# Performance work log

Measured on AMD Instinct MI355X. Metric: run time of the kernel, lower is better.

The kernel has to match this reference:

```python
import jax, jax.numpy as jnp
import numpy as np

B, S, H, E, V, T, OOV = 32, 400, 256, 300, 50000, 20, 50


def setup_inputs() -> dict:
    key = jax.random.key(0)
    ks = jax.random.split(key, 24)
    g = lambda k, sh, scale=0.02: jax.random.normal(k, sh, dtype=jnp.float32) * scale
    return {
        "enc_hidden": jax.random.normal(ks[0], (B, S, 2 * H), dtype=jnp.float32),
        "h0": jax.random.normal(ks[1], (B, H), dtype=jnp.float32),
        "c0": jax.random.normal(ks[2], (B, H), dtype=jnp.float32),
        "embedding": g(ks[3], (V, E), 1.0),
        "W_enc": g(ks[4], (2 * H, H)),
        "W_dec": g(ks[5], (H, H)),
        "w_cov": g(ks[6], (H,)),
        "v_attn": g(ks[7], (H,)),
        "W_ih": g(ks[8], (E, 4 * H)),
        "W_hh": g(ks[9], (H, 4 * H)),
        "b_lstm": jnp.zeros((4 * H,), jnp.float32),
        "W_out1": g(ks[10], (3 * H, H)),
        "b_out1": jnp.zeros((H,), jnp.float32),
        "W_out2": g(ks[11], (H, V)),
        "b_out2": jnp.zeros((V,), jnp.float32),
        "w_h": g(ks[12], (2 * H, 1)),
        "w_s": g(ks[13], (H, 1)),
        "w_x": g(ks[14], (E, 1)),
        "b_x": jnp.zeros((1,), jnp.float32),
        "dec_input": jax.random.randint(ks[15], (B, T), 0, V),
        "enc_input_ext": jax.random.randint(ks[16], (B, S), 0, V + OOV),
        "enc_pad_mask": jnp.ones((B, S), dtype=bool),
        "max_oov_len": OOV,
    }


def reference(enc_hidden, h0, c0, embedding, W_enc, W_dec, w_cov, v_attn,
              W_ih, W_hh, b_lstm, W_out1, b_out1, W_out2, b_out2,
              w_h, w_s, w_x, b_x, dec_input, enc_input_ext, enc_pad_mask,
              max_oov_len):
    b, s, two_h = enc_hidden.shape
    enc_feat = enc_hidden @ W_enc  # [B,S,H], precomputed attention keys
    batch_idx = jnp.arange(b)[:, None]
    NEG = jnp.float32(-1e9)

    def step(carry, x_t):
        h, c, cov = carry
        emb = embedding[x_t]  # [B,E]
        # LSTM cell
        gates = emb @ W_ih + h @ W_hh + b_lstm
        i, f, gg, o = jnp.split(gates, 4, axis=-1)
        c = jax.nn.sigmoid(f) * c + jax.nn.sigmoid(i) * jnp.tanh(gg)
        h = jax.nn.sigmoid(o) * jnp.tanh(c)
        # coverage attention over encoder states
        e = jnp.tanh(enc_feat + (h @ W_dec)[:, None, :] + cov[..., None] * w_cov) @ v_attn  # [B,S]
        e = jnp.where(enc_pad_mask, e, NEG)
        attn = jax.nn.softmax(e, axis=-1)
        context = jnp.einsum('bs,bsd->bd', attn, enc_hidden)  # [B,2H]
        cov = cov + attn
        # vocab distribution
        out = jnp.concatenate([h, context], axis=-1) @ W_out1 + b_out1
        vocab_dist = jax.nn.softmax(out @ W_out2 + b_out2, axis=-1)  # [B,V]
        # pointer-generator gate
        p_gen = jax.nn.sigmoid(context @ w_h + h @ w_s + emb @ w_x + b_x)  # [B,1]
        vocab_dist = p_gen * vocab_dist
        weighted_attn = (1.0 - p_gen) * attn
        # extend vocab and scatter-add copy probabilities
        ext = jnp.concatenate(
            [vocab_dist, jnp.zeros((b, max_oov_len), vocab_dist.dtype)], axis=-1)
        final = ext.at[batch_idx, enc_input_ext].add(weighted_attn)
        return (h, c, cov), (final, attn, cov)

    cov0 = jnp.zeros((b, s), jnp.float32)
    _, (finals, attns, covs) = jax.lax.scan(step, (h0, c0, cov0), dec_input.T)
    # stack with time on the last axis, as in the torch module
    return (jnp.moveaxis(finals, 0, -1),
            jnp.moveaxis(attns, 0, -1),
            jnp.moveaxis(covs, 0, -1))
```

## Files before the change

kernel.cpp:

```cpp
#include <hip/hip_runtime.h>
#include <hip/hip_bf16.h>

#define B_    32
#define S_    400
#define H_    256
#define E_    300
#define V_    50000
#define T_    20
#define VE_   50050
#define TB_   640
#define VPAD_ 50048
#define FIN_  32032000
#define NB_   16
#define SC_   25

typedef __attribute__((ext_vector_type(8))) short bf16x8;
typedef __attribute__((ext_vector_type(4))) float f32x4;

__device__ __forceinline__ float sigmoid_f(float x){ return 1.f/(1.f+__expf(-x)); }
__device__ __forceinline__ float tanh_f(float x){ return 1.f - 2.f/(__expf(2.f*x)+1.f); }

__device__ __forceinline__ float bf2f(unsigned short u){
  union { unsigned int i; float f; } x; x.i = ((unsigned int)u) << 16; return x.f;
}
__device__ __forceinline__ unsigned short f2bf(float f){
  union { __hip_bfloat16 h; unsigned short u; } x; x.h = __float2bfloat16(f); return x.u;
}

__device__ __forceinline__ void st_dev(float* p, float v){
  __hip_atomic_store(p, v, __ATOMIC_RELAXED, __HIP_MEMORY_SCOPE_AGENT);
}
__device__ __forceinline__ float ld_dev(const float* p){
  return __hip_atomic_load(p, __ATOMIC_RELAXED, __HIP_MEMORY_SCOPE_AGENT);
}

__device__ __forceinline__ void rowbar(int* cnt, int* gen, int target){
  __syncthreads();
  if (threadIdx.x == 0){
    asm volatile("s_waitcnt vmcnt(0)" ::: "memory");
    int old = __hip_atomic_fetch_add(cnt, 1, __ATOMIC_RELAXED, __HIP_MEMORY_SCOPE_AGENT);
    if (old == NB_ - 1){
      __hip_atomic_store(cnt, 0, __ATOMIC_RELAXED, __HIP_MEMORY_SCOPE_AGENT);
      asm volatile("s_waitcnt vmcnt(0)" ::: "memory");
      __hip_atomic_fetch_add(gen, 1, __ATOMIC_RELAXED, __HIP_MEMORY_SCOPE_AGENT);
    } else {
      while (__hip_atomic_load(gen, __ATOMIC_RELAXED, __HIP_MEMORY_SCOPE_AGENT) < target){
        __builtin_amdgcn_s_sleep(1);
      }
    }
  }
  __syncthreads();
}


__global__ __launch_bounds__(256) void kc1(const float* __restrict__ in,
                                           __hip_bfloat16* __restrict__ out){
  size_t g = (size_t)blockIdx.x*256 + threadIdx.x;
  float4 f = ((const float4*)in)[g];
  size_t o = g*4;
  out[o+0] = __float2bfloat16(f.x);
  out[o+1] = __float2bfloat16(f.y);
  out[o+2] = __float2bfloat16(f.z);
  out[o+3] = __float2bfloat16(f.w);
}

__global__ __launch_bounds__(256) void kT(const float* __restrict__ in,
                                          __hip_bfloat16* __restrict__ out, int R, int C){
  __shared__ float tile[32][33];
  int tx = threadIdx.x & 31, ty = threadIdx.x >> 5;
  int c = blockIdx.x*32 + tx;
  #pragma unroll
  for (int i = 0; i < 4; ++i){
    int r = blockIdx.y*32 + ty + i*8;
    if (r < R && c < C) tile[ty + i*8][tx] = in[(size_t)r*C + c];
  }
  __syncthreads();
  int r2 = blockIdx.y*32 + tx;
  #pragma unroll
  for (int i = 0; i < 4; ++i){
    int c2 = blockIdx.x*32 + ty + i*8;
    if (r2 < R && c2 < C) out[(size_t)c2*R + r2] = __float2bfloat16(tile[tx][ty + i*8]);
  }
}

__global__ __launch_bounds__(256) void kpair(const float* __restrict__ in,
                                             unsigned short* __restrict__ out, int N){
  int g = blockIdx.x*256 + threadIdx.x;
  int k = g / N, n = g % N;
  out[(size_t)(k >> 1)*(2*N) + n*2 + (k & 1)] = f2bf(in[g]);
}

__global__ __launch_bounds__(256) void k1(const float* __restrict__ emb,
                                          const int* __restrict__ dec,
                                          const float* __restrict__ W_ih,
                                          const float* __restrict__ b_lstm,
                                          float* __restrict__ pre_ih){
  int tid = threadIdx.x;
  int n0 = blockIdx.x*64, m0 = blockIdx.y*64;
  __shared__ float A_s[64][21];
  __shared__ float B_s[20][65];
  __shared__ int gid_s[64];
  if (tid < 64){
    int r = m0 + tid;
    gid_s[tid] = dec[(r & 31)*20 + (r >> 5)];
  }
  float acc[4][4] = {};
  int ty = tid >> 4, tx = tid & 15;
  for (int kc = 0; kc < 15; ++kc){
    __syncthreads();
    for (int e = tid; e < 1280; e += 256){
      int row = e / 20, kk = e % 20;
      A_s[row][kk] = emb[(size_t)gid_s[row]*300 + kc*20 + kk];
    }
    for (int e = tid; e < 1280; e += 256){
      int kk = e >> 6, c = e & 63;
      B_s[kk][c] = W_ih[(size_t)(kc*20 + kk)*1024 + n0 + c];
    }
    __syncthreads();
    #pragma unroll
    for (int kk = 0; kk < 20; ++kk){
      float av[4], bv[4];
      #pragma unroll
      for (int i = 0; i < 4; ++i) av[i] = A_s[ty*4 + i][kk];
      #pragma unroll
      for (int j = 0; j < 4; ++j) bv[j] = B_s[kk][tx*4 + j];
      #pragma unroll
      for (int i = 0; i < 4; ++i)
        #pragma unroll
        for (int j = 0; j < 4; ++j) acc[i][j] += av[i]*bv[j];
    }
  }
  #pragma unroll
  for (int i = 0; i < 4; ++i)
    #pragma unroll
    for (int j = 0; j < 4; ++j){
      int rr = m0 + ty*4 + i, cc = n0 + tx*4 + j;
      pre_ih[(size_t)rr*1024 + cc] = acc[i][j] + b_lstm[cc];
    }
}

__global__ __launch_bounds__(64) void k1b(const float* __restrict__ emb,
                                          const int* __restrict__ dec,
                                          const float* __restrict__ w_x,
                                          const float* __restrict__ b_x,
                                          float* __restrict__ pre_x){
  int r = blockIdx.x, lane = threadIdx.x;
  int gid = dec[(r & 31)*20 + (r >> 5)];
  float p = 0.f;
  for (int k = lane; k < 300; k += 64) p += emb[(size_t)gid*300 + k]*w_x[k];
  #pragma unroll
  for (int off = 32; off > 0; off >>= 1) p += __shfl_xor(p, off);
  if (lane == 0) pre_x[r] = p + b_x[0];
}

__global__ __launch_bounds__(256) void k2(const __hip_bfloat16* __restrict__ Abf,
                                          const __hip_bfloat16* __restrict__ Bt,
                                          __hip_bfloat16* __restrict__ Cbf){
  int tid = threadIdx.x;
  int lane = tid & 63, wave = tid >> 6;
  int wm = wave >> 1, wn = wave & 1;
  int n0 = blockIdx.x*128, m0 = blockIdx.y*128;
  __shared__ __align__(16) unsigned short A_s[128][40];
  __shared__ __align__(16) unsigned short B_s[128][40];
  f32x4 acc[4][4];
  #pragma unroll
  for (int i = 0; i < 4; ++i)
    #pragma unroll
    for (int j = 0; j < 4; ++j) acc[i][j] = (f32x4){0.f,0.f,0.f,0.f};
  int cg = tid & 3;
  for (int kc = 0; kc < 16; ++kc){
    __syncthreads();
    #pragma unroll
    for (int rr = 0; rr < 2; ++rr){
      int row = (tid >> 2) + rr*64;
      *(float4*)&A_s[row][cg*8] = *(const float4*)(Abf + (size_t)(m0+row)*512 + kc*32 + cg*8);
      *(float4*)&B_s[row][cg*8] = *(const float4*)(Bt  + (size_t)(n0+row)*512 + kc*32 + cg*8);
    }
    __syncthreads();
    bf16x8 af[4], bfr[4];
    #pragma unroll
    for (int mt = 0; mt < 4; ++mt)
      af[mt] = *(const bf16x8*)&A_s[wm*64 + mt*16 + (lane & 15)][(lane >> 4)*8];
    #pragma unroll
    for (int nt = 0; nt < 4; ++nt)
      bfr[nt] = *(const bf16x8*)&B_s[wn*64 + nt*16 + (lane & 15)][(lane >> 4)*8];
    #pragma unroll
    for (int mt = 0; mt < 4; ++mt)
      #pragma unroll
      for (int nt = 0; nt < 4; ++nt)
        acc[mt][nt] = __builtin_amdgcn_mfma_f32_16x16x32_bf16(af[mt], bfr[nt], acc[mt][nt], 0, 0, 0);
  }
  int lm = lane & 15, lq = lane >> 4;
  #pragma unroll
  for (int mt = 0; mt < 4; ++mt)
    #pragma unroll
    for (int nt = 0; nt < 4; ++nt){
      int vv = n0 + wn*64 + nt*16 + lm;
      #pragma unroll
      for (int rg = 0; rg < 4; ++rg){
        int r = m0 + wm*64 + mt*16 + lq*4 + rg;
        Cbf[(size_t)r*256 + vv] = __float2bfloat16(acc[mt][nt][rg]);
      }
    }
}

__global__ __launch_bounds__(256) void krec(
    const float* __restrict__ h0, const float* __restrict__ c0,
    const unsigned short* __restrict__ Whh2,
    const unsigned short* __restrict__ Wd2,
    const float* __restrict__ w_cov, const float* __restrict__ v_attn,
    const float* __restrict__ pre_ih, const __hip_bfloat16* __restrict__ enc_feat,
    const float* __restrict__ enc_hidden,
    float* __restrict__ H_all, float* __restrict__ exps_g,
    float* __restrict__ Zatt, float* __restrict__ ctxp, int* bar)
{
  const int bx = blockIdx.x;
  const int b = bx >> 4, jj = bx & 15;
  const int tid = threadIdx.x;
  const int lane = tid & 63, wave = tid >> 6;
  const int s0 = jj*SC_;

  __shared__ __align__(16) unsigned short eh_s[SC_][512];
  __shared__ __align__(16) unsigned short ef_s[SC_][256];
  __shared__ float h_sh[256], hdec_sh[256], vat[256], wcv[256], g_lds[256];
  __shared__ float c_loc[16];
  __shared__ float covf[32], exps_l[32];
  __shared__ float zprev_sh;

  for (int e = tid; e < SC_*128; e += 256){
    int row = e >> 7, c4 = e & 127;
    float4 f = *(const float4*)(enc_hidden + ((size_t)(b*400 + s0 + row))*512 + c4*4);
    unsigned int lo = ((unsigned int)f2bf(f.y) << 16) | f2bf(f.x);
    unsigned int hi = ((unsigned int)f2bf(f.w) << 16) | f2bf(f.z);
    *(unsigned int*)&eh_s[row][c4*4]     = lo;
    *(unsigned int*)&eh_s[row][c4*4 + 2] = hi;
  }
  for (int e = tid; e < SC_*32; e += 256){
    int row = e >> 5, c8 = e & 31;
    *(float4*)&ef_s[row][c8*8] =
      *(const float4*)(enc_feat + ((size_t)(b*400 + s0 + row))*256 + c8*8);
  }
  vat[tid] = v_attn[tid];
  wcv[tid] = w_cov[tid];
  h_sh[tid] = h0[b*256 + tid];
  if (tid < 16) c_loc[tid] = c0[b*256 + jj*16 + tid];
  if (tid < 32) { covf[tid] = 0.f; exps_l[tid] = 0.f; }

  const int col = tid & 63;
  const int g = col >> 4, ci = col & 15;
  const int gcol = g*256 + jj*16 + ci;
  const int kq = tid >> 6;
  ushort2 wreg[32];
  #pragma unroll
  for (int pp = 0; pp < 32; ++pp)
    wreg[pp] = *(const ushort2*)(Whh2 + ((size_t)(kq*32 + pp))*2048 + gcol*2);

  __syncthreads();

  int* cnt = bar + b*16;
  int* gen = cnt + 1;

  for (int t = 0; t < T_; ++t){
    const int r = t*32 + b;
    {
      float acc = 0.f;
      #pragma unroll
      for (int pp = 0; pp < 32; ++pp){
        float2 h2 = *(const float2*)&h_sh[kq*64 + pp*2];
        acc += h2.x*bf2f(wreg[pp].x) + h2.y*bf2f(wreg[pp].y);
      }
      if (kq == 0) acc += pre_ih[(size_t)r*1024 + gcol];
      g_lds[tid] = acc;
    }
    __syncthreads();
    if (tid < 16){
      float gi = 0.f, gf = 0.f, gg = 0.f, go = 0.f;
      #pragma unroll
      for (int kq2 = 0; kq2 < 4; ++kq2){
        gi += g_lds[kq2*64 +  0 + tid];
        gf += g_lds[kq2*64 + 16 + tid];
        gg += g_lds[kq2*64 + 32 + tid];
        go += g_lds[kq2*64 + 48 + tid];
      }
      float cn = sigmoid_f(gf)*c_loc[tid] + sigmoid_f(gi)*tanh_f(gg);
      c_loc[tid] = cn;
      st_dev(&H_all[(size_t)r*256 + jj*16 + tid], sigmoid_f(go)*tanh_f(cn));
    }
    rowbar(cnt, gen, t + 1);
    h_sh[tid] = ld_dev(&H_all[(size_t)r*256 + tid]);
    if (tid == 0 && t > 0) zprev_sh = ld_dev(&Zatt[r - 32]);
    __syncthreads();
    if (t > 0 && tid < SC_) covf[tid] += exps_l[tid] / zprev_sh;
    {
      float acc = 0.f;
      const unsigned short* wp = Wd2 + tid*2;
      #pragma unroll 16
      for (int pp = 0; pp < 128; ++pp){
        ushort2 w2 = *(const ushort2*)(wp + (size_t)pp*512);
        acc += h_sh[pp*2]*bf2f(w2.x) + h_sh[pp*2 + 1]*bf2f(w2.y);
      }
      hdec_sh[tid] = acc;
    }
    __syncthreads();
    for (int sl = wave; sl < SC_; sl += 4){
      const float cw = covf[sl];
      float part = 0.f;
      #pragma unroll
      for (int q = 0; q < 4; ++q){
        int k = lane + q*64;
        float x = bf2f(ef_s[sl][k]) + hdec_sh[k] + cw*wcv[k];
        part += vat[k]*tanh_f(x);
      }
      #pragma unroll
      for (int off = 32; off > 0; off >>= 1) part += __shfl_xor(part, off);
      if (lane == 0){
        float ev = __expf(part);
        exps_l[sl] = ev;
        exps_g[(size_t)r*400 + s0 + sl] = ev;
      }
    }
    __syncthreads();
    if (tid == 0){
      float z = 0.f;
      #pragma unroll
      for (int q = 0; q < SC_; ++q) z += exps_l[q];
      atomicAdd(&Zatt[r], z);
    }
    #pragma unroll
    for (int hh = 0; hh < 2; ++hh){
      int d = tid + hh*256;
      float acc = 0.f;
      #pragma unroll
      for (int sl = 0; sl < SC_; ++sl) acc += exps_l[sl]*bf2f(eh_s[sl][d]);
      ctxp[((size_t)r*16 + jj)*512 + d] = acc;
    }
    __syncthreads();
  }
}

__global__ __launch_bounds__(256) void k3a(const float* __restrict__ Zatt,
                                           const float* __restrict__ ctxp,
                                           const float* __restrict__ H_all,
                                           const float* __restrict__ w_h,
                                           const float* __restrict__ w_s,
                                           const float* __restrict__ pre_x,
                                           float* __restrict__ CAT,
                                           float* __restrict__ pgen){
  int r = blockIdx.x, tid = threadIdx.x;
  __shared__ float red[256];
  float invz = 1.f/Zatt[r];
  float hv = H_all[(size_t)r*256 + tid];
  CAT[(size_t)r*768 + tid] = hv;
  float a0 = 0.f, a1 = 0.f;
  const float* p = ctxp + (size_t)r*16*512;
  #pragma unroll
  for (int jj = 0; jj < 16; ++jj){
    a0 += p[jj*512 + tid];
    a1 += p[jj*512 + 256 + tid];
  }
  float cv0 = a0*invz;
  float cv1 = a1*invz;
  CAT[(size_t)r*768 + 256 + tid] = cv0;
  CAT[(size_t)r*768 + 512 + tid] = cv1;
  float pg = hv*w_s[tid] + cv0*w_h[tid] + cv1*w_h[tid + 256];
  red[tid] = pg; __syncthreads();
  for (int st = 128; st > 0; st >>= 1){
    if (tid < st) red[tid] += red[tid + st];
    __syncthreads();
  }
  if (tid == 0) pgen[r] = sigmoid_f(red[0] + pre_x[r]);
}

__global__ __launch_bounds__(256) void k3b(const float* __restrict__ exps_g,
                                           const float* __restrict__ Zatt,
                                           float* __restrict__ attns,
                                           float* __restrict__ covs){
  __shared__ float tA[256*20];
  __shared__ float tC[256*20];
  int tid = threadIdx.x;
  int g0 = blockIdx.x*256;
  int g = g0 + tid;
  int b = g / 400, s = g % 400;
  float cum = 0.f;
  for (int t = 0; t < T_; ++t){
    int r = t*32 + b;
    float a = exps_g[(size_t)r*400 + s] / Zatt[r];
    cum += a;
    tA[tid*20 + t] = a;
    tC[tid*20 + t] = cum;
  }
  __syncthreads();
  size_t base = (size_t)g0*20;
  for (int e = tid; e < 5120; e += 256){
    attns[base + e] = tA[e];
    covs[base + e]  = tC[e];
  }
}

__global__ __launch_bounds__(256) void k4(const float* __restrict__ CAT,
                                          const float* __restrict__ W_out1,
                                          const float* __restrict__ b_out1,
                                          __hip_bfloat16* __restrict__ OUTb){
  int tid = threadIdx.x;
  int n0 = blockIdx.x*64, m0 = blockIdx.y*64;
  __shared__ float A_s[64][17];
  __shared__ float B_s[16][65];
  float acc[4][4] = {};
  int ty = tid >> 4, tx = tid & 15;
  for (int kc = 0; kc < 48; ++kc){
    __syncthreads();
    for (int e = tid; e < 1024; e += 256){
      int row = e >> 4, kk = e & 15;
      A_s[row][kk] = CAT[(size_t)(m0 + row)*768 + kc*16 + kk];
    }
    for (int e = tid; e < 1024; e += 256){
      int kk = e >> 6, c = e & 63;
      B_s[kk][c] = W_out1[(size_t)(kc*16 + kk)*256 + n0 + c];
    }
    __syncthreads();
    #pragma unroll
    for (int kk = 0; kk < 16; ++kk){
      float av[4], bv[4];
      #pragma unroll
      for (int i = 0; i < 4; ++i) av[i] = A_s[ty*4 + i][kk];
      #pragma unroll
      for (int j = 0; j < 4; ++j) bv[j] = B_s[kk][tx*4 + j];
      #pragma unroll
      for (int i = 0; i < 4; ++i)
        #pragma unroll
        for (int j = 0; j < 4; ++j) acc[i][j] += av[i]*bv[j];
    }
  }
  #pragma unroll
  for (int i = 0; i < 4; ++i)
    #pragma unroll
    for (int j = 0; j < 4; ++j){
      int rr = m0 + ty*4 + i, cc = n0 + tx*4 + j;
      OUTb[(size_t)rr*256 + cc] = __float2bfloat16(acc[i][j] + b_out1[cc]);
    }
}

__global__ __launch_bounds__(256) void k5(const __hip_bfloat16* __restrict__ OUTb,
                                          const __hip_bfloat16* __restrict__ W2t,
                                          const float* __restrict__ b_out2,
                                          __hip_bfloat16* __restrict__ temp,
                                          float* __restrict__ Zsum){
  int tid = threadIdx.x;
  int lane = tid & 63, wave = tid >> 6;
  int wm = wave >> 1, wn = wave & 1;
  int n0 = blockIdx.y*128, m0 = blockIdx.x*128;
  __shared__ __align__(16) unsigned short A_s[128][40];
  __shared__ __align__(16) unsigned short B_s[128][40];
  f32x4 acc[4][4];
  #pragma unroll
  for (int i = 0; i < 4; ++i)
    #pragma unroll
    for (int j = 0; j < 4; ++j) acc[i][j] = (f32x4){0.f,0.f,0.f,0.f};
  int cg = tid & 3;
  for (int kc = 0; kc < 8; ++kc){
    __syncthreads();
    #pragma unroll
    for (int rr = 0; rr < 2; ++rr){
      int row = (tid >> 2) + rr*64;
      *(float4*)&A_s[row][cg*8] = *(const float4*)(OUTb + (size_t)(m0 + row)*256 + kc*32 + cg*8);
      int v = n0 + row;
      float4 bv = make_float4(0.f, 0.f, 0.f, 0.f);
      if (v < V_) bv = *(const float4*)(W2t + (size_t)v*256 + kc*32 + cg*8);
      *(float4*)&B_s[row][cg*8] = bv;
    }
    __syncthreads();
    bf16x8 af[4], bfr[4];
    #pragma unroll
    for (int mt = 0; mt < 4; ++mt)
      af[mt] = *(const bf16x8*)&A_s[wm*64 + mt*16 + (lane & 15)][(lane >> 4)*8];
    #pragma unroll
    for (int nt = 0; nt < 4; ++nt)
      bfr[nt] = *(const bf16x8*)&B_s[wn*64 + nt*16 + (lane & 15)][(lane >> 4)*8];
    #pragma unroll
    for (int mt = 0; mt < 4; ++mt)
      #pragma unroll
      for (int nt = 0; nt < 4; ++nt)
        acc[mt][nt] = __builtin_amdgcn_mfma_f32_16x16x32_bf16(af[mt], bfr[nt], acc[mt][nt], 0, 0, 0);
  }
  int lm = lane & 15, lq = lane >> 4;
  float rowsum[4][4];
  #pragma unroll
  for (int mt = 0; mt < 4; ++mt)
    #pragma unroll
    for (int rg = 0; rg < 4; ++rg) rowsum[mt][rg] = 0.f;
  #pragma unroll
  for (int mt = 0; mt < 4; ++mt)
    #pragma unroll
    for (int nt = 0; nt < 4; ++nt){
      int vv = n0 + wn*64 + nt*16 + lm;
      float b2 = (vv < V_) ? b_out2[vv] : 0.f;
      #pragma unroll
      for (int rg = 0; rg < 4; ++rg){
        int r = m0 + wm*64 + mt*16 + lq*4 + rg;
        float e = __expf(acc[mt][nt][rg] + b2);
        temp[(size_t)r*VPAD_ + vv] = __float2bfloat16(e);
        if (vv >= V_) e = 0.f;
        rowsum[mt][rg] += e;
      }
    }
  #pragma unroll
  for (int mt = 0; mt < 4; ++mt)
    #pragma unroll
    for (int rg = 0; rg < 4; ++rg){
      float s = rowsum[mt][rg];
      s += __shfl_xor(s, 1); s += __shfl_xor(s, 2);
      s += __shfl_xor(s, 4); s += __shfl_xor(s, 8);
      if (lm == 0){
        int r = m0 + wm*64 + mt*16 + lq*4 + rg;
        atomicAdd(&Zsum[r], s);
      }
    }
}

__global__ __launch_bounds__(256) void k6(const __hip_bfloat16* __restrict__ temp,
                                          const float* __restrict__ pgen,
                                          const float* __restrict__ Zsum,
                                          float* __restrict__ finals){
  int b = blockIdx.y, cb = blockIdx.x, tid = threadIdx.x;
  int v0 = cb*512;
  __shared__ float tile[20][513];
  __shared__ float ssc[20];
  if (tid < 20){ int r = tid*32 + b; ssc[tid] = pgen[r]/Zsum[r]; }
  __syncthreads();
  for (int e = tid; e < 1280; e += 256){
    int tt = e >> 6, c8 = e & 63;
    int v = v0 + c8*8;
    float sc = ssc[tt];
    const __hip_bfloat16* src = temp + (size_t)(tt*32 + b)*VPAD_ + v;
    if (v + 7 < V_){
      float4 raw = *(const float4*)src;
      const unsigned short* u = (const unsigned short*)&raw;
      #pragma unroll
      for (int j = 0; j < 8; ++j) tile[tt][c8*8 + j] = bf2f(u[j])*sc;
    } else {
      #pragma unroll
      for (int j = 0; j < 8; ++j)
        tile[tt][c8*8 + j] = (v + j < V_) ? __bfloat162float(src[j])*sc : 0.f;
    }
  }
  __syncthreads();
  int wlim = (VE_ - v0)*20; if (wlim > 10240) wlim = 10240;
  float* dst = finals + (size_t)b*1001000 + (size_t)v0*20;
  for (int e = tid; e < wlim; e += 256){
    dst[e] = tile[e % 20][e / 20];
  }
}

__global__ __launch_bounds__(320) void k7(const float* __restrict__ exps_g,
                                          const float* __restrict__ Zatt,
                                          const float* __restrict__ pgen,
                                          const int* __restrict__ ext,
                                          float* __restrict__ finals){
  int tid = threadIdx.x;
  int g = blockIdx.x*16 + tid/20;
  int t = tid % 20;
  int b = g / 400, s = g % 400;
  int r = t*32 + b;
  int idx = ext[g];
  float w = (1.f - pgen[r])*exps_g[(size_t)r*400 + s]/Zatt[r];
  atomicAdd(finals + (size_t)b*1001000 + (size_t)idx*20 + t, w);
}

extern "C" void kernel_launch(void* const* d_in, const int* in_sizes, int n_in,
                              void* d_out, int out_size, void* d_ws, size_t ws_size,
                              hipStream_t stream){
  const float* enc_hidden = (const float*)d_in[0];
  const float* h0         = (const float*)d_in[1];
  const float* c0         = (const float*)d_in[2];
  const float* embedding  = (const float*)d_in[3];
  const float* W_enc      = (const float*)d_in[4];
  const float* W_dec      = (const float*)d_in[5];
  const float* w_cov      = (const float*)d_in[6];
  const float* v_attn     = (const float*)d_in[7];
  const float* W_ih       = (const float*)d_in[8];
  const float* W_hh       = (const float*)d_in[9];
  const float* b_lstm     = (const float*)d_in[10];
  const float* W_out1     = (const float*)d_in[11];
  const float* b_out1     = (const float*)d_in[12];
  const float* W_out2     = (const float*)d_in[13];
  const float* b_out2     = (const float*)d_in[14];
  const float* w_h        = (const float*)d_in[15];
  const float* w_s        = (const float*)d_in[16];
  const float* w_x        = (const float*)d_in[17];
  const float* b_x        = (const float*)d_in[18];
  const int*   dec_input  = (const int*)d_in[19];
  const int*   enc_ext    = (const int*)d_in[20];

  float* out    = (float*)d_out;
  float* finals = out;
  float* attns  = out + FIN_;
  float* covs   = out + FIN_ + 256000;

  char* w = (char*)d_ws;
  auto alloc = [&](size_t n){ char* p = w; w += (n + 255) & ~(size_t)255; return p; };
  int*   bar      = (int*)  alloc(32*64);
  float* Zsum     = (float*)alloc((size_t)TB_*4);
  float* Zatt     = (float*)alloc((size_t)TB_*4);
  float* pre_ih   = (float*)alloc((size_t)TB_*1024*4);
  float* pre_x    = (float*)alloc((size_t)TB_*4);
  unsigned short* Whh2 = (unsigned short*)alloc((size_t)256*1024*2);
  unsigned short* Wd2  = (unsigned short*)alloc((size_t)256*256*2);
  __hip_bfloat16* enc_bf   = (__hip_bfloat16*)alloc((size_t)12800*512*2);
  __hip_bfloat16* WencT    = (__hip_bfloat16*)alloc((size_t)256*512*2);
  __hip_bfloat16* W2t      = (__hip_bfloat16*)alloc((size_t)V_*256*2);
  __hip_bfloat16* enc_feat = (__hip_bfloat16*)alloc((size_t)12800*256*2);
  float* H_all    = (float*)alloc((size_t)TB_*256*4);
  float* exps_g   = (float*)alloc((size_t)TB_*400*4);
  float* CAT      = (float*)alloc((size_t)TB_*768*4);
  float* pgen     = (float*)alloc((size_t)TB_*4);
  __hip_bfloat16* OUTb = (__hip_bfloat16*)alloc((size_t)TB_*256*2);
  __hip_bfloat16* temp = (__hip_bfloat16*)alloc((size_t)TB_*VPAD_*2);
  float* ctxp     = (float*)temp;

  hipMemsetAsync(bar, 0, 32*64, stream);
  hipMemsetAsync(Zsum, 0, (size_t)TB_*4, stream);
  hipMemsetAsync(Zatt, 0, (size_t)TB_*4, stream);

  kc1<<<6400, 256, 0, stream>>>(enc_hidden, enc_bf);
  kT <<<dim3(8, 16), 256, 0, stream>>>(W_enc, WencT, 512, 256);
  kT <<<dim3(1563, 8), 256, 0, stream>>>(W_out2, W2t, 256, V_);
  kpair<<<1024, 256, 0, stream>>>(W_hh, Whh2, 1024);
  kpair<<<256, 256, 0, stream>>>(W_dec, Wd2, 256);
  k1 <<<dim3(16, 10), 256, 0, stream>>>(embedding, dec_input, W_ih, b_lstm, pre_ih);
  k1b<<<640, 64, 0, stream>>>(embedding, dec_input, w_x, b_x, pre_x);
  k2 <<<dim3(2, 100), 256, 0, stream>>>(enc_bf, WencT, enc_feat);
  krec<<<512, 256, 0, stream>>>(h0, c0, Whh2, Wd2, w_cov, v_attn, pre_ih,
                                enc_feat, enc_hidden,
                                H_all, exps_g, Zatt, ctxp, bar);
  k3a<<<640, 256, 0, stream>>>(Zatt, ctxp, H_all, w_h, w_s, pre_x, CAT, pgen);
  k3b<<<50, 256, 0, stream>>>(exps_g, Zatt, attns, covs);
  k4 <<<dim3(4, 10), 256, 0, stream>>>(CAT, W_out1, b_out1, OUTb);
  k5 <<<dim3(5, 391), 256, 0, stream>>>(OUTb, W2t, b_out2, temp, Zsum);
  k6 <<<dim3(98, 32), 256, 0, stream>>>(temp, pgen, Zsum, finals);
  k7 <<<800, 320, 0, stream>>>(exps_g, Zatt, pgen, enc_ext, finals);
}
```

Before: 945.0 us.

## Restructure recurrent kernel: shuffle-based gate reduction, split W_dec matvec, monotonic barrier

Recurrent LSTM-attention kernel reorganised. Gate partial sums are now reduced with wave shuffles instead of an LDS round trip and an extra block barrier. The h@W_dec matvec is split across the 16 blocks of a batch row: each block computes a partial from its own 16 hidden units before the cross-block barrier and the partials are summed afterwards. This removes the full 256x256 matvec from the post-barrier critical path. The row barrier becomes a monotonic counter without a generation reset, and double-buffered exp history drops the trailing __syncthreads. The cost is 16 extra global loads per thread per step and more scratch traffic.

```diff
diff --git a/kernel.cpp b/kernel.cpp
--- a/kernel.cpp
+++ b/kernel.cpp
@@ -34,19 +34,13 @@
   return __hip_atomic_load(p, __ATOMIC_RELAXED, __HIP_MEMORY_SCOPE_AGENT);
 }
 
-__device__ __forceinline__ void rowbar(int* cnt, int* gen, int target){
+__device__ __forceinline__ void rowbar(int* cnt, int target){
   __syncthreads();
   if (threadIdx.x == 0){
     asm volatile("s_waitcnt vmcnt(0)" ::: "memory");
-    int old = __hip_atomic_fetch_add(cnt, 1, __ATOMIC_RELAXED, __HIP_MEMORY_SCOPE_AGENT);
-    if (old == NB_ - 1){
-      __hip_atomic_store(cnt, 0, __ATOMIC_RELAXED, __HIP_MEMORY_SCOPE_AGENT);
-      asm volatile("s_waitcnt vmcnt(0)" ::: "memory");
-      __hip_atomic_fetch_add(gen, 1, __ATOMIC_RELAXED, __HIP_MEMORY_SCOPE_AGENT);
-    } else {
-      while (__hip_atomic_load(gen, __ATOMIC_RELAXED, __HIP_MEMORY_SCOPE_AGENT) < target){
-        __builtin_amdgcn_s_sleep(1);
-      }
+    __hip_atomic_fetch_add(cnt, 1, __ATOMIC_RELAXED, __HIP_MEMORY_SCOPE_AGENT);
+    while (__hip_atomic_load(cnt, __ATOMIC_RELAXED, __HIP_MEMORY_SCOPE_AGENT) < target){
+      __builtin_amdgcn_s_sleep(1);
     }
   }
   __syncthreads();
@@ -212,7 +206,8 @@
     const float* __restrict__ pre_ih, const __hip_bfloat16* __restrict__ enc_feat,
     const float* __restrict__ enc_hidden,
     float* __restrict__ H_all, float* __restrict__ exps_g,
-    float* __restrict__ Zatt, float* __restrict__ ctxp, int* bar)
+    float* __restrict__ Zatt, float* __restrict__ ctxp,
+    float* __restrict__ hdecp, int* bar)
 {
   const int bx = blockIdx.x;
   const int b = bx >> 4, jj = bx & 15;
@@ -222,10 +217,10 @@
 
   __shared__ __align__(16) unsigned short eh_s[SC_][512];
   __shared__ __align__(16) unsigned short ef_s[SC_][256];
-  __shared__ float h_sh[256], hdec_sh[256], vat[256], wcv[256], g_lds[256];
-  __shared__ float c_loc[16];
-  __shared__ float covf[32], exps_l[32];
-  __shared__ float zprev_sh;
+  __shared__ float h_sh[256], hdec_sh[256], vat[256], wcv[256];
+  __shared__ float h_loc[16];
+  __shared__ float covf[32], ehist[2][32];
+  __shared__ float invZ_sh;
 
   for (int e = tid; e < SC_*128; e += 256){
     int row = e >> 7, c4 = e & 127;
@@ -243,67 +238,75 @@
   vat[tid] = v_attn[tid];
   wcv[tid] = w_cov[tid];
   h_sh[tid] = h0[b*256 + tid];
-  if (tid < 16) c_loc[tid] = c0[b*256 + jj*16 + tid];
-  if (tid < 32) { covf[tid] = 0.f; exps_l[tid] = 0.f; }
-
-  const int col = tid & 63;
-  const int g = col >> 4, ci = col & 15;
-  const int gcol = g*256 + jj*16 + ci;
-  const int kq = tid >> 6;
+  if (tid < 32) covf[tid] = 0.f;
+
+  const int kq = lane & 3, cl = (lane >> 2) & 3, gt = lane >> 4;
+  const int ci = wave*4 + cl;
+  const int gcol = gt*256 + jj*16 + ci;
   ushort2 wreg[32];
   #pragma unroll
   for (int pp = 0; pp < 32; ++pp)
     wreg[pp] = *(const ushort2*)(Whh2 + ((size_t)(kq*32 + pp))*2048 + gcol*2);
+  ushort2 wdreg[8];
+  #pragma unroll
+  for (int p = 0; p < 8; ++p)
+    wdreg[p] = *(const ushort2*)(Wd2 + ((size_t)(jj*8 + p))*512 + tid*2);
+  float c_reg = c0[b*256 + jj*16 + ci];
 
   __syncthreads();
 
   int* cnt = bar + b*16;
-  int* gen = cnt + 1;
-
+
+  #pragma unroll 1
   for (int t = 0; t < T_; ++t){
     const int r = t*32 + b;
+    float acc = (kq == 0) ? pre_ih[(size_t)r*1024 + gcol] : 0.f;
+    #pragma unroll
+    for (int pp = 0; pp < 32; ++pp){
+      float2 h2 = *(const float2*)&h_sh[kq*64 + pp*2];
+      acc += h2.x*bf2f(wreg[pp].x) + h2.y*bf2f(wreg[pp].y);
+    }
+    acc += __shfl_xor(acc, 1);
+    acc += __shfl_xor(acc, 2);
     {
-      float acc = 0.f;
-      #pragma unroll
-      for (int pp = 0; pp < 32; ++pp){
-        float2 h2 = *(const float2*)&h_sh[kq*64 + pp*2];
-        acc += h2.x*bf2f(wreg[pp].x) + h2.y*bf2f(wreg[pp].y);
+      int base = lane & 12;
+      float gi = __shfl(acc, base);
+      float gf = __shfl(acc, base + 16);
+      float gG = __shfl(acc, base + 32);
+      float go = __shfl(acc, base + 48);
+      float cn = sigmoid_f(gf)*c_reg + sigmoid_f(gi)*tanh_f(gG);
+      c_reg = cn;
+      float hv = sigmoid_f(go)*tanh_f(cn);
+      if ((lane & 51) == 0){
+        st_dev(&H_all[(size_t)r*256 + jj*16 + ci], hv);
+        h_loc[ci] = hv;
       }
-      if (kq == 0) acc += pre_ih[(size_t)r*1024 + gcol];
-      g_lds[tid] = acc;
-    }
-    __syncthreads();
-    if (tid < 16){
-      float gi = 0.f, gf = 0.f, gg = 0.f, go = 0.f;
-      #pragma unroll
-      for (int kq2 = 0; kq2 < 4; ++kq2){
-        gi += g_lds[kq2*64 +  0 + tid];
-        gf += g_lds[kq2*64 + 16 + tid];
-        gg += g_lds[kq2*64 + 32 + tid];
-        go += g_lds[kq2*64 + 48 + tid];
-      }
-      float cn = sigmoid_f(gf)*c_loc[tid] + sigmoid_f(gi)*tanh_f(gg);
-      c_loc[tid] = cn;
-      st_dev(&H_all[(size_t)r*256 + jj*16 + tid], sigmoid_f(go)*tanh_f(cn));
-    }
-    rowbar(cnt, gen, t + 1);
-    h_sh[tid] = ld_dev(&H_all[(size_t)r*256 + tid]);
-    if (tid == 0 && t > 0) zprev_sh = ld_dev(&Zatt[r - 32]);
-    __syncthreads();
-    if (t > 0 && tid < SC_) covf[tid] += exps_l[tid] / zprev_sh;
+    }
+    __syncthreads();
     {
-      float acc = 0.f;
-      const unsigned short* wp = Wd2 + tid*2;
-      #pragma unroll 16
-      for (int pp = 0; pp < 128; ++pp){
-        ushort2 w2 = *(const ushort2*)(wp + (size_t)pp*512);
-        acc += h_sh[pp*2]*bf2f(w2.x) + h_sh[pp*2 + 1]*bf2f(w2.y);
-      }
-      hdec_sh[tid] = acc;
-    }
-    __syncthreads();
+      float pd = 0.f;
+      #pragma unroll
+      for (int p = 0; p < 8; ++p)
+        pd += h_loc[p*2]*bf2f(wdreg[p].x) + h_loc[p*2 + 1]*bf2f(wdreg[p].y);
+      st_dev(&hdecp[((size_t)r*16 + jj)*256 + tid], pd);
+    }
+    rowbar(cnt, NB_*(t + 1));
+    {
+      float hfull = ld_dev(&H_all[(size_t)r*256 + tid]);
+      float hd = 0.f;
+      #pragma unroll
+      for (int j2 = 0; j2 < 16; ++j2)
+        hd += ld_dev(&hdecp[((size_t)r*16 + j2)*256 + tid]);
+      h_sh[tid] = hfull;
+      hdec_sh[tid] = hd;
+      if (tid == 0 && t > 0) invZ_sh = 1.f/ld_dev(&Zatt[r - 32]);
+    }
+    __syncthreads();
+    float* ecur = ehist[t & 1];
+    const float* eprev = ehist[(t ^ 1) & 1];
     for (int sl = wave; sl < SC_; sl += 4){
-      const float cw = covf[sl];
+      float cw = covf[sl];
+      if (t > 0) cw += eprev[sl]*invZ_sh;
       float part = 0.f;
       #pragma unroll
       for (int q = 0; q < 4; ++q){
@@ -314,8 +317,9 @@
       #pragma unroll
       for (int off = 32; off > 0; off >>= 1) part += __shfl_xor(part, off);
       if (lane == 0){
+        covf[sl] = cw;
         float ev = __expf(part);
-        exps_l[sl] = ev;
+        ecur[sl] = ev;
         exps_g[(size_t)r*400 + s0 + sl] = ev;
       }
     }
@@ -323,18 +327,17 @@
     if (tid == 0){
       float z = 0.f;
       #pragma unroll
-      for (int q = 0; q < SC_; ++q) z += exps_l[q];
+      for (int q = 0; q < SC_; ++q) z += ecur[q];
       atomicAdd(&Zatt[r], z);
     }
     #pragma unroll
     for (int hh = 0; hh < 2; ++hh){
       int d = tid + hh*256;
-      float acc = 0.f;
-      #pragma unroll
-      for (int sl = 0; sl < SC_; ++sl) acc += exps_l[sl]*bf2f(eh_s[sl][d]);
-      ctxp[((size_t)r*16 + jj)*512 + d] = acc;
-    }
-    __syncthreads();
+      float a2 = 0.f;
+      #pragma unroll
+      for (int sl = 0; sl < SC_; ++sl) a2 += ecur[sl]*bf2f(eh_s[sl][d]);
+      ctxp[((size_t)r*16 + jj)*512 + d] = a2;
+    }
   }
 }
 
@@ -616,6 +619,7 @@
   __hip_bfloat16* OUTb = (__hip_bfloat16*)alloc((size_t)TB_*256*2);
   __hip_bfloat16* temp = (__hip_bfloat16*)alloc((size_t)TB_*VPAD_*2);
   float* ctxp     = (float*)temp;
+  float* hdecp    = (float*)((char*)temp + (size_t)TB_*16*512*4);
 
   hipMemsetAsync(bar, 0, 32*64, stream);
   hipMemsetAsync(Zsum, 0, (size_t)TB_*4, stream);
@@ -631,7 +635,7 @@
   k2 <<<dim3(2, 100), 256, 0, stream>>>(enc_bf, WencT, enc_feat);
   krec<<<512, 256, 0, stream>>>(h0, c0, Whh2, Wd2, w_cov, v_attn, pre_ih,
                                 enc_feat, enc_hidden,
-                                H_all, exps_g, Zatt, ctxp, bar);
+                                H_all, exps_g, Zatt, ctxp, hdecp, bar);
   k3a<<<640, 256, 0, stream>>>(Zatt, ctxp, H_all, w_h, w_s, pre_x, CAT, pgen);
   k3b<<<50, 256, 0, stream>>>(exps_g, Zatt, attns, covs);
   k4 <<<dim3(4, 10), 256, 0, stream>>>(CAT, W_out1, b_out1, OUTb);
```

Result: faster. 904.7 us (-4.3%).
